# Performance work log

Hardware: AMD Instinct MI355X
Metric: run time of the kernel (lower is better)

The kernel has to match this reference:

```python
import jax, jax.numpy as jnp
import numpy as np

B, S, E, H = 4, 2048, 1024, 8
D = E // H  # head_dim = 128


def setup_inputs() -> dict:
    key = jax.random.key(0)
    ks = jax.random.split(key, 7)
    scale = 1.0 / np.sqrt(D)
    return {
        "sequences": jax.random.normal(ks[0], (B, S, E), dtype=jnp.float32),
        # per-head Linear weights, torch layout [out, in] stacked over heads
        "Wq": jax.random.normal(ks[1], (H, D, D), dtype=jnp.float32) * scale,
        "Wk": jax.random.normal(ks[2], (H, D, D), dtype=jnp.float32) * scale,
        "Wv": jax.random.normal(ks[3], (H, D, D), dtype=jnp.float32) * scale,
        "bq": jax.random.normal(ks[4], (H, D), dtype=jnp.float32) * scale,
        "bk": jax.random.normal(ks[5], (H, D), dtype=jnp.float32) * scale,
        "bv": jax.random.normal(ks[6], (H, D), dtype=jnp.float32) * scale,
    }


def reference(sequences, Wq, Wk, Wv, bq, bk, bv):
    # split feature dim into heads: [B,S,H,D]
    xh = sequences.reshape(B, S, H, D)
    # torch Linear: y = x @ W.T + b  ->  contract input dim d with W[h, o, d]
    q = jnp.einsum("bshd,hod->bsho", xh, Wq) + bq
    k = jnp.einsum("bshd,hod->bsho", xh, Wk) + bk
    v = jnp.einsum("bshd,hod->bsho", xh, Wv) + bv
    # NOTE: original scales by 1/sqrt(num_heads), not 1/sqrt(head_dim)
    scores = jnp.einsum("bshd,bthd->bhst", q, k) / jnp.sqrt(jnp.float32(H))
    attn = jax.nn.softmax(scores, axis=-1)  # [B,H,S,S]
    out = jnp.einsum("bhst,bthd->bshd", attn, v)
    # hstack over heads == reshape back to [B,S,E]
    return out.reshape(B, S, E)
```

## Files before the change

kernel.cpp:

```cpp
#include <hip/hip_runtime.h>
#include <hip/hip_bf16.h>

#define B_ 4
#define S_ 2048
#define E_ 1024
#define H_ 8
#define D_ 128

using f16x8 = __attribute__((ext_vector_type(8))) _Float16;
using f32x4 = __attribute__((ext_vector_type(4))) float;

__device__ __forceinline__ ushort f2h_bits(float f) {
    union { _Float16 h; ushort u; } cv; cv.h = (_Float16)f; return cv.u;
}
__device__ __forceinline__ float max3f(float a, float b, float c) {
    return fmaxf(fmaxf(a, b), c);
}
__device__ __forceinline__ f16x8 pack8(const float* __restrict__ p) {
    float4 f0 = *(const float4*)p;
    float4 f1 = *(const float4*)(p + 4);
    f16x8 r;
    r[0] = (_Float16)f0.x; r[1] = (_Float16)f0.y;
    r[2] = (_Float16)f0.z; r[3] = (_Float16)f0.w;
    r[4] = (_Float16)f1.x; r[5] = (_Float16)f1.y;
    r[6] = (_Float16)f1.z; r[7] = (_Float16)f1.w;
    return r;
}

__device__ __forceinline__ void gll16(const ushort* g, ushort* l) {
    __builtin_amdgcn_global_load_lds(
        (const __attribute__((address_space(1))) unsigned int*)g,
        (__attribute__((address_space(3))) unsigned int*)l, 16, 0, 0);
}

__global__ __launch_bounds__(256) void kv_proj(
    const float* __restrict__ seq,
    const float* __restrict__ Wk, const float* __restrict__ Wv,
    const float* __restrict__ bk, const float* __restrict__ bv,
    ushort* __restrict__ ko, ushort* __restrict__ vo)
{
    constexpr int TS = 136;
    __shared__ ushort Tk[128 * TS];
    __shared__ ushort Tv[128 * TS];
    const int m0 = blockIdx.x * 128, h = blockIdx.y;
    const int tid = threadIdx.x, lane = tid & 63, w = tid >> 6;
    const int l16 = lane & 15, quad = lane >> 4;

    f16x8 a[2][4];
    #pragma unroll
    for (int mt = 0; mt < 2; ++mt)
        #pragma unroll
        for (int ks = 0; ks < 4; ++ks)
            a[mt][ks] = pack8(&seq[(size_t)(m0 + w * 32 + mt * 16 + l16) * E_
                                   + h * D_ + ks * 32 + quad * 8]);

    {
        const float* W = Wk + (size_t)h * D_ * D_;
        f32x4 acc[2][8];
        #pragma unroll
        for (int mt = 0; mt < 2; ++mt)
            #pragma unroll
            for (int nt = 0; nt < 8; ++nt) { f32x4 z = {0.f,0.f,0.f,0.f}; acc[mt][nt] = z; }
        #pragma unroll
        for (int ks = 0; ks < 4; ++ks)
            #pragma unroll
            for (int nt = 0; nt < 8; ++nt) {
                f16x8 bfr = pack8(&W[(size_t)(nt * 16 + l16) * D_ + ks * 32 + quad * 8]);
                #pragma unroll
                for (int mt = 0; mt < 2; ++mt)
                    acc[mt][nt] = __builtin_amdgcn_mfma_f32_16x16x32_f16(
                        a[mt][ks], bfr, acc[mt][nt], 0, 0, 0);
            }
        #pragma unroll
        for (int nt = 0; nt < 8; ++nt) {
            int o = nt * 16 + l16;
            float bias = bk[h * D_ + o];
            #pragma unroll
            for (int mt = 0; mt < 2; ++mt)
                #pragma unroll
                for (int r = 0; r < 4; ++r) {
                    int row = w * 32 + mt * 16 + quad * 4 + r;
                    Tk[row * TS + (o ^ (quad << 3))] = f2h_bits(acc[mt][nt][r] + bias);
                }
        }
    }
    {
        const float* W = Wv + (size_t)h * D_ * D_;
        f32x4 acc[2][8];
        #pragma unroll
        for (int mt = 0; mt < 2; ++mt)
            #pragma unroll
            for (int nt = 0; nt < 8; ++nt) { f32x4 z = {0.f,0.f,0.f,0.f}; acc[mt][nt] = z; }
        #pragma unroll
        for (int ks = 0; ks < 4; ++ks)
            #pragma unroll
            for (int nt = 0; nt < 8; ++nt) {
                f16x8 bfr = pack8(&W[(size_t)(nt * 16 + l16) * D_ + ks * 32 + quad * 8]);
                #pragma unroll
                for (int mt = 0; mt < 2; ++mt)
                    acc[mt][nt] = __builtin_amdgcn_mfma_f32_16x16x32_f16(
                        a[mt][ks], bfr, acc[mt][nt], 0, 0, 0);
            }
        #pragma unroll
        for (int nt = 0; nt < 8; ++nt) {
            int o = nt * 16 + l16;
            float bias = bv[h * D_ + o];
            #pragma unroll
            for (int mt = 0; mt < 2; ++mt)
                #pragma unroll
                for (int r = 0; r < 4; ++r) {
                    int row = w * 32 + mt * 16 + quad * 4 + r;
                    Tv[o * TS + row] = f2h_bits(acc[mt][nt][r] + bias);
                }
        }
    }
    __syncthreads();

    #pragma unroll
    for (int i = 0; i < 8; ++i) {
        int idx = tid + i * 256;
        int row = idx >> 4, c8 = (idx & 15) * 8;
        int lk = c8 ^ ((row & 7) << 3);
        uint4 dk = *(uint4*)&Tk[row * TS + (lk ^ (((row >> 2) & 3) << 3))];
        int m = m0 + row, bi = m >> 11, s = m & (S_ - 1);
        *(uint4*)&ko[(((size_t)bi * H_ + h) * S_ + s) * D_ + c8] = dk;
        uint4 dv = *(uint4*)&Tv[row * TS + (c8 ^ ((row & 7) << 3))];
        int mg = m0 + c8, bv_i = mg >> 11, s0 = mg & (S_ - 1);
        *(uint4*)&vo[(((size_t)bv_i * H_ + h) * D_ + row) * S_ + s0] = dv;
    }
}

__global__ __launch_bounds__(512, 4) void attn(
    const float* __restrict__ seq, const float* __restrict__ Wq,
    const float* __restrict__ bq,
    const ushort* __restrict__ kg, const ushort* __restrict__ vtg,
    float* __restrict__ out)
{
    constexpr int NT = S_ / 64;
    __shared__ alignas(16) ushort Kbuf[2][64 * 128];
    __shared__ alignas(16) ushort Vbuf[2][128 * 64];
    __shared__ alignas(16) ushort Pbuf[128 * 64];

    const int L = blockIdx.x + 16 * blockIdx.y + 128 * blockIdx.z;
    const int c = L & 7, t = L >> 3;
    const int g = c * 4 + (t & 3);
    const int h = g & 7, bi = g >> 3;
    const int m0 = (t >> 2) * 128;

    const int bh = bi * H_ + h;
    const int tid = threadIdx.x, lane = tid & 63, w = tid >> 6;
    const int l16 = lane & 15, quad = lane >> 4;
    const int swz = l16 & 7;
    const ushort* kbase = kg + (size_t)bh * S_ * D_;
    const ushort* vbase = vtg + (size_t)bh * D_ * S_;
    const float qscale = 0.35355339059327373f * 1.4426950408889634f;

    #pragma unroll
    for (int ci = 0; ci < 2; ++ci) {
        int i = w * 2 + ci;
        gll16(vbase + (size_t)(i * 8 + (lane >> 3)) * S_ + (lane & 7) * 8,
              &Vbuf[0][0] + i * 512);
    }

    ushort* const Qs = &Kbuf[0][0];
    {
        f16x8 xa[4];
        #pragma unroll
        for (int ks = 0; ks < 4; ++ks)
            xa[ks] = pack8(&seq[((size_t)bi * S_ + m0 + w * 16 + l16) * E_
                                + h * D_ + ks * 32 + quad * 8]);
        f32x4 qacc[8];
        #pragma unroll
        for (int nt = 0; nt < 8; ++nt) { f32x4 z = {0.f,0.f,0.f,0.f}; qacc[nt] = z; }
        const float* W = Wq + (size_t)h * D_ * D_;
        #pragma unroll
        for (int ks = 0; ks < 4; ++ks)
            #pragma unroll
            for (int nt = 0; nt < 8; ++nt) {
                f16x8 bfr = pack8(&W[(size_t)(nt * 16 + l16) * D_ + ks * 32 + quad * 8]);
                qacc[nt] = __builtin_amdgcn_mfma_f32_16x16x32_f16(
                    xa[ks], bfr, qacc[nt], 0, 0, 0);
            }
        #pragma unroll
        for (int nt = 0; nt < 8; ++nt) {
            int o = nt * 16 + l16;
            float bias = bq[h * D_ + o];
            #pragma unroll
            for (int r = 0; r < 4; ++r) {
                int row = w * 16 + quad * 4 + r;
                Qs[row * 128 + (o ^ (quad << 3))] =
                    f2h_bits((qacc[nt][r] + bias) * qscale);
            }
        }
    }
    __syncthreads();

    f16x8 qf[4];
    #pragma unroll
    for (int ks = 0; ks < 4; ++ks)
        qf[ks] = *(const f16x8*)&Qs[(w * 16 + l16) * 128
                                    + ks * 32 + ((quad ^ (l16 >> 2)) << 3)];
    __syncthreads();

    #pragma unroll
    for (int ci = 0; ci < 2; ++ci) {
        int i = w * 2 + ci;
        gll16(kbase + i * 512 + lane * 8, &Kbuf[0][0] + i * 512);
    }

    f32x4 o_acc[8];
    #pragma unroll
    for (int nt = 0; nt < 8; ++nt) { f32x4 z = {0.f,0.f,0.f,0.f}; o_acc[nt] = z; }
    float m_prev = -1e30f, l_lane = 0.f;

    __syncthreads();

    ushort* const prow = &Pbuf[(w * 16 + l16) * 64];

    #pragma unroll 2
    for (int j = 0; j < NT; ++j) {
        const int cur = j & 1;
        const ushort* KL = &Kbuf[cur][0];
        const ushort* VL = &Vbuf[cur][0];

        if (j + 1 < NT) {
            const ushort* kt = kbase + (size_t)(j + 1) * 64 * 128;
            const ushort* vt = vbase + (j + 1) * 64;
            ushort* kd = &Kbuf[cur ^ 1][0];
            ushort* vd = &Vbuf[cur ^ 1][0];
            #pragma unroll
            for (int ci = 0; ci < 2; ++ci) {
                int i = w * 2 + ci;
                gll16(kt + i * 512 + lane * 8, kd + i * 512);
                gll16(vt + (size_t)(i * 8 + (lane >> 3)) * S_ + (lane & 7) * 8,
                      vd + i * 512);
            }
        }

        f32x4 sacc[4];
        #pragma unroll
        for (int nt = 0; nt < 4; ++nt) { f32x4 z = {0.f,0.f,0.f,0.f}; sacc[nt] = z; }
        __builtin_amdgcn_s_setprio(1);
        #pragma unroll
        for (int ks = 0; ks < 4; ++ks)
            #pragma unroll
            for (int nt = 0; nt < 4; ++nt) {
                f16x8 kf = *(const f16x8*)&KL[(nt * 16 + l16) * 128
                                              + (((ks * 4 + quad) ^ swz) << 3)];
                sacc[nt] = __builtin_amdgcn_mfma_f32_16x16x32_f16(
                    kf, qf[ks], sacc[nt], 0, 0, 0);
            }
        __builtin_amdgcn_s_setprio(0);

        {
            float v0 = max3f(sacc[0][0], sacc[0][1], sacc[0][2]);
            float v1 = max3f(sacc[0][3], sacc[1][0], sacc[1][1]);
            float v2 = max3f(sacc[1][2], sacc[1][3], sacc[2][0]);
            float v3 = max3f(sacc[2][1], sacc[2][2], sacc[2][3]);
            float v4 = max3f(sacc[3][0], sacc[3][1], sacc[3][2]);
            float mx = fmaxf(max3f(v0, v1, v2), max3f(v3, v4, sacc[3][3]));
            mx = fmaxf(mx, __shfl_xor(mx, 16));
            mx = fmaxf(mx, __shfl_xor(mx, 32));
            if (__any(mx > m_prev + 8.0f)) {
                float mnew  = fmaxf(m_prev, mx);
                float alpha = exp2f(m_prev - mnew);
                #pragma unroll
                for (int nt = 0; nt < 8; ++nt)
                    #pragma unroll
                    for (int r = 0; r < 4; ++r) o_acc[nt][r] *= alpha;
                l_lane *= alpha;
                m_prev = mnew;
            }
            #pragma unroll
            for (int nt = 0; nt < 4; ++nt) {
                float e0 = exp2f(sacc[nt][0] - m_prev);
                float e1 = exp2f(sacc[nt][1] - m_prev);
                float e2 = exp2f(sacc[nt][2] - m_prev);
                float e3 = exp2f(sacc[nt][3] - m_prev);
                auto p01 = __builtin_amdgcn_cvt_pkrtz(e0, e1);
                auto p23 = __builtin_amdgcn_cvt_pkrtz(e2, e3);
                int G = 2 * nt + (quad >> 1);
                *(uint2*)&prow[((G ^ swz) << 3) + ((quad & 1) << 2)] =
                    make_uint2(__builtin_bit_cast(uint, p01),
                               __builtin_bit_cast(uint, p23));
                l_lane += (float)p01[0] + (float)p01[1] + (float)p23[0] + (float)p23[1];
            }
        }

        __builtin_amdgcn_s_setprio(1);
        #pragma unroll
        for (int ks = 0; ks < 2; ++ks) {
            f16x8 pb = *(const f16x8*)&prow[((ks * 4 + quad) ^ swz) << 3];
            #pragma unroll
            for (int nt = 0; nt < 8; ++nt) {
                f16x8 vf = *(const f16x8*)&VL[(nt * 16 + l16) * 64
                                              + (((ks * 4 + quad) ^ swz) << 3)];
                o_acc[nt] = __builtin_amdgcn_mfma_f32_16x16x32_f16(
                    vf, pb, o_acc[nt], 0, 0, 0);
            }
        }
        __builtin_amdgcn_s_setprio(0);

        __syncthreads();
    }

    {
        float l = l_lane;
        l += __shfl_xor(l, 16);
        l += __shfl_xor(l, 32);
        float rinv = 1.0f / l;
        const int q = m0 + w * 16 + l16;
        #pragma unroll
        for (int nt = 0; nt < 8; ++nt) {
            float4 o;
            o.x = o_acc[nt][0] * rinv;
            o.y = o_acc[nt][1] * rinv;
            o.z = o_acc[nt][2] * rinv;
            o.w = o_acc[nt][3] * rinv;
            *(float4*)&out[((size_t)bi * S_ + q) * E_ + h * D_ + nt * 16 + quad * 4] = o;
        }
    }
}

extern "C" void kernel_launch(void* const* d_in, const int* in_sizes, int n_in,
                              void* d_out, int out_size, void* d_ws, size_t ws_size,
                              hipStream_t stream) {
    const float* seq = (const float*)d_in[0];
    const float* Wq  = (const float*)d_in[1];
    const float* Wk  = (const float*)d_in[2];
    const float* Wv  = (const float*)d_in[3];
    const float* bq  = (const float*)d_in[4];
    const float* bk  = (const float*)d_in[5];
    const float* bv  = (const float*)d_in[6];

    const size_t per = (size_t)B_ * H_ * S_ * D_;
    if (ws_size < 2 * per * sizeof(ushort)) return;
    ushort* kws  = (ushort*)d_ws;
    ushort* vtws = kws + per;

    kv_proj<<<dim3(B_ * S_ / 128, H_), 256, 0, stream>>>(
        seq, Wk, Wv, bk, bv, kws, vtws);
    attn<<<dim3(16, 8, 4), 512, 0, stream>>>(
        seq, Wq, bq, kws, vtws, (float*)d_out);
}
```

Measured before the change: 247.9 us.

## Halve attention KV tile to 32 keys to raise occupancy

The flash-attention KV tile shrinks from 64 to 32 keys, and LDS becomes one shared 40KB buffer instead of about 80KB. Launch bounds change from 4 to 8 blocks per CU so more waves can be resident. The V-transpose store and the P/V swizzles are reworked for the narrower 32-column rows, and the V prefetch before the Q projection is dropped. In exchange there are twice as many loop iterations, each with a barrier and a max/rescale step, and less MFMA work to hide latency per iteration.

```diff
diff --git a/kernel.cpp b/kernel.cpp
--- a/kernel.cpp
+++ b/kernel.cpp
@@ -124,22 +124,28 @@
         uint4 dk = *(uint4*)&Tk[row * TS + (lk ^ (((row >> 2) & 3) << 3))];
         int m = m0 + row, bi = m >> 11, s = m & (S_ - 1);
         *(uint4*)&ko[(((size_t)bi * H_ + h) * S_ + s) * D_ + c8] = dk;
-        uint4 dv = *(uint4*)&Tv[row * TS + (c8 ^ ((row & 7) << 3))];
-        int mg = m0 + c8, bv_i = mg >> 11, s0 = mg & (S_ - 1);
+        int cc = idx & 15;
+        int s2v = (row ^ (row >> 2)) & 3;
+        uint4 dv = *(uint4*)&Tv[row * TS + (((cc & 12) | ((cc & 3) ^ s2v)) << 3)];
+        int mg = m0 + cc * 8, bv_i = mg >> 11, s0 = mg & (S_ - 1);
         *(uint4*)&vo[(((size_t)bv_i * H_ + h) * D_ + row) * S_ + s0] = dv;
     }
 }
 
-__global__ __launch_bounds__(512, 4) void attn(
+__global__ __launch_bounds__(512, 8) void attn(
     const float* __restrict__ seq, const float* __restrict__ Wq,
     const float* __restrict__ bq,
     const ushort* __restrict__ kg, const ushort* __restrict__ vtg,
     float* __restrict__ out)
 {
-    constexpr int NT = S_ / 64;
-    __shared__ alignas(16) ushort Kbuf[2][64 * 128];
-    __shared__ alignas(16) ushort Vbuf[2][128 * 64];
-    __shared__ alignas(16) ushort Pbuf[128 * 64];
+    constexpr int NT = S_ / 32;
+    __shared__ alignas(16) ushort smem[20480];
+    ushort* const Kb0 = smem;
+    ushort* const Kb1 = smem + 4096;
+    ushort* const Vb0 = smem + 8192;
+    ushort* const Vb1 = smem + 12288;
+    ushort* const Pbuf = smem + 16384;
+    ushort* const Qs = smem;
 
     const int L = blockIdx.x + 16 * blockIdx.y + 128 * blockIdx.z;
     const int c = L & 7, t = L >> 3;
@@ -151,18 +157,11 @@
     const int tid = threadIdx.x, lane = tid & 63, w = tid >> 6;
     const int l16 = lane & 15, quad = lane >> 4;
     const int swz = l16 & 7;
+    const int s2 = (l16 ^ (l16 >> 2)) & 3;
     const ushort* kbase = kg + (size_t)bh * S_ * D_;
     const ushort* vbase = vtg + (size_t)bh * D_ * S_;
     const float qscale = 0.35355339059327373f * 1.4426950408889634f;
 
-    #pragma unroll
-    for (int ci = 0; ci < 2; ++ci) {
-        int i = w * 2 + ci;
-        gll16(vbase + (size_t)(i * 8 + (lane >> 3)) * S_ + (lane & 7) * 8,
-              &Vbuf[0][0] + i * 512);
-    }
-
-    ushort* const Qs = &Kbuf[0][0];
     {
         f16x8 xa[4];
         #pragma unroll
@@ -202,11 +201,9 @@
                                     + ks * 32 + ((quad ^ (l16 >> 2)) << 3)];
     __syncthreads();
 
-    #pragma unroll
-    for (int ci = 0; ci < 2; ++ci) {
-        int i = w * 2 + ci;
-        gll16(kbase + i * 512 + lane * 8, &Kbuf[0][0] + i * 512);
-    }
+    gll16(kbase + w * 512 + lane * 8, Kb0 + w * 512);
+    gll16(vbase + (size_t)(w * 16 + (lane >> 2)) * S_ + (lane & 3) * 8,
+          Vb0 + w * 512);
 
     f32x4 o_acc[8];
     #pragma unroll
@@ -215,36 +212,32 @@
 
     __syncthreads();
 
-    ushort* const prow = &Pbuf[(w * 16 + l16) * 64];
+    ushort* const prow = &Pbuf[(w * 16 + l16) * 32];
 
     #pragma unroll 2
     for (int j = 0; j < NT; ++j) {
         const int cur = j & 1;
-        const ushort* KL = &Kbuf[cur][0];
-        const ushort* VL = &Vbuf[cur][0];
+        const ushort* KL = cur ? Kb1 : Kb0;
+        const ushort* VL = cur ? Vb1 : Vb0;
 
         if (j + 1 < NT) {
-            const ushort* kt = kbase + (size_t)(j + 1) * 64 * 128;
-            const ushort* vt = vbase + (j + 1) * 64;
-            ushort* kd = &Kbuf[cur ^ 1][0];
-            ushort* vd = &Vbuf[cur ^ 1][0];
-            #pragma unroll
-            for (int ci = 0; ci < 2; ++ci) {
-                int i = w * 2 + ci;
-                gll16(kt + i * 512 + lane * 8, kd + i * 512);
-                gll16(vt + (size_t)(i * 8 + (lane >> 3)) * S_ + (lane & 7) * 8,
-                      vd + i * 512);
-            }
-        }
-
-        f32x4 sacc[4];
-        #pragma unroll
-        for (int nt = 0; nt < 4; ++nt) { f32x4 z = {0.f,0.f,0.f,0.f}; sacc[nt] = z; }
+            const ushort* kt = kbase + (size_t)(j + 1) * 32 * 128;
+            const ushort* vt = vbase + (j + 1) * 32;
+            ushort* kd = cur ? Kb0 : Kb1;
+            ushort* vd = cur ? Vb0 : Vb1;
+            gll16(kt + w * 512 + lane * 8, kd + w * 512);
+            gll16(vt + (size_t)(w * 16 + (lane >> 2)) * S_ + (lane & 3) * 8,
+                  vd + w * 512);
+        }
+
+        f32x4 sacc[2];
+        #pragma unroll
+        for (int nt = 0; nt < 2; ++nt) { f32x4 z = {0.f,0.f,0.f,0.f}; sacc[nt] = z; }
         __builtin_amdgcn_s_setprio(1);
         #pragma unroll
         for (int ks = 0; ks < 4; ++ks)
             #pragma unroll
-            for (int nt = 0; nt < 4; ++nt) {
+            for (int nt = 0; nt < 2; ++nt) {
                 f16x8 kf = *(const f16x8*)&KL[(nt * 16 + l16) * 128
                                               + (((ks * 4 + quad) ^ swz) << 3)];
                 sacc[nt] = __builtin_amdgcn_mfma_f32_16x16x32_f16(
@@ -255,10 +248,7 @@
         {
             float v0 = max3f(sacc[0][0], sacc[0][1], sacc[0][2]);
             float v1 = max3f(sacc[0][3], sacc[1][0], sacc[1][1]);
-            float v2 = max3f(sacc[1][2], sacc[1][3], sacc[2][0]);
-            float v3 = max3f(sacc[2][1], sacc[2][2], sacc[2][3]);
-            float v4 = max3f(sacc[3][0], sacc[3][1], sacc[3][2]);
-            float mx = fmaxf(max3f(v0, v1, v2), max3f(v3, v4, sacc[3][3]));
+            float mx = max3f(v0, v1, fmaxf(sacc[1][2], sacc[1][3]));
             mx = fmaxf(mx, __shfl_xor(mx, 16));
             mx = fmaxf(mx, __shfl_xor(mx, 32));
             if (__any(mx > m_prev + 8.0f)) {
@@ -272,7 +262,7 @@
                 m_prev = mnew;
             }
             #pragma unroll
-            for (int nt = 0; nt < 4; ++nt) {
+            for (int nt = 0; nt < 2; ++nt) {
                 float e0 = exp2f(sacc[nt][0] - m_prev);
                 float e1 = exp2f(sacc[nt][1] - m_prev);
                 float e2 = exp2f(sacc[nt][2] - m_prev);
@@ -280,7 +270,7 @@
                 auto p01 = __builtin_amdgcn_cvt_pkrtz(e0, e1);
                 auto p23 = __builtin_amdgcn_cvt_pkrtz(e2, e3);
                 int G = 2 * nt + (quad >> 1);
-                *(uint2*)&prow[((G ^ swz) << 3) + ((quad & 1) << 2)] =
+                *(uint2*)&prow[((G ^ s2) << 3) + ((quad & 1) << 2)] =
                     make_uint2(__builtin_bit_cast(uint, p01),
                                __builtin_bit_cast(uint, p23));
                 l_lane += (float)p01[0] + (float)p01[1] + (float)p23[0] + (float)p23[1];
@@ -288,13 +278,12 @@
         }
 
         __builtin_amdgcn_s_setprio(1);
-        #pragma unroll
-        for (int ks = 0; ks < 2; ++ks) {
-            f16x8 pb = *(const f16x8*)&prow[((ks * 4 + quad) ^ swz) << 3];
+        {
+            f16x8 pb = *(const f16x8*)&prow[((quad ^ s2) << 3)];
             #pragma unroll
             for (int nt = 0; nt < 8; ++nt) {
-                f16x8 vf = *(const f16x8*)&VL[(nt * 16 + l16) * 64
-                                              + (((ks * 4 + quad) ^ swz) << 3)];
+                f16x8 vf = *(const f16x8*)&VL[(nt * 16 + l16) * 32
+                                              + ((quad ^ s2) << 3)];
                 o_acc[nt] = __builtin_amdgcn_mfma_f32_16x16x32_f16(
                     vf, pb, o_acc[nt], 0, 0, 0);
             }
```

Result: slower. 454.3 us (+83.2%).
